# Kernel optimization log

Measured on AMD Instinct MI355X. Metric: run time of the kernel, lower is better.

## Reference

```python
import jax, jax.numpy as jnp
import numpy as np

N = 50000   # nodes
E = 800000  # edges
G = 64      # graphs
D_IN = 128
D_OUT = 64
HID = 2 * D_OUT  # 128, hidden width of non-final layers
EPS = 1e-5


def _seg_sum(v, idx, n):
    return jax.ops.segment_sum(v, idx, num_segments=n)


def _gcn(x, W, b, src, dst, n):
    # GCNConv with default add_self_loops=True, edge_weight=1, sym norm
    xw = x @ W                                            # [N, out]
    deg = _seg_sum(jnp.ones(src.shape[0], x.dtype), dst, n) + 1.0  # +1 self loop
    dis = jax.lax.rsqrt(deg)                              # deg^{-1/2}, deg>=1
    norm = dis[src] * dis[dst]                            # [E]
    agg = _seg_sum(norm[:, None] * xw[src], dst, n)       # gather-scale-scatter
    return agg + (dis * dis)[:, None] * xw + b            # self-loop term + bias


def _mpnn_layer(x, src, dst, edge_attr, gw, gb, ew, eb, n):
    h = _gcn(x, gw, gb, src, dst, n)
    e = jax.nn.relu(edge_attr[:, None] * ew + eb)         # Linear(1,out).relu per edge
    msg = h[src] + e                                      # message = x_j + edge_attr
    cnt = _seg_sum(jnp.ones(src.shape[0], x.dtype), dst, n)
    return _seg_sum(msg, dst, n) / jnp.clip(cnt, 1.0)[:, None]  # scatter-mean


def _ln(x, g, b):
    # node-wise LayerNorm over feature dim
    mu = x.mean(-1, keepdims=True)
    var = x.var(-1, keepdims=True)
    return (x - mu) * jax.lax.rsqrt(var + EPS) * g + b


def setup_inputs() -> dict:
    key = jax.random.key(0)
    ks = jax.random.split(key, 24)
    x = jax.random.normal(ks[0], (N, D_IN), jnp.float32)
    edge_index = jax.random.randint(ks[1], (2, E), 0, N, dtype=jnp.int64)
    edge_attr = jax.random.uniform(ks[2], (E,), jnp.float32)
    batch = jnp.sort(jax.random.randint(ks[3], (N,), 0, G, dtype=jnp.int64))

    def lin(k, fan_in, shape):
        return jax.random.uniform(k, shape, jnp.float32, -1.0, 1.0) / np.sqrt(fan_in)

    # layer 0: in 128 -> 128; layer 1: 128 -> 128; layer 2: 128 -> 64
    inp = {
        "x": x, "edge_index": edge_index, "edge_attr": edge_attr, "batch": batch,
        "gcn_w0": lin(ks[4], D_IN, (D_IN, HID)),  "gcn_b0": jnp.zeros((HID,), jnp.float32),
        "edge_w0": lin(ks[5], 1, (HID,)),          "edge_b0": lin(ks[6], 1, (HID,)),
        "ln_g0": jnp.ones((HID,), jnp.float32),   "ln_b0": jnp.zeros((HID,), jnp.float32),
        "gcn_w1": lin(ks[7], HID, (HID, HID)),    "gcn_b1": jnp.zeros((HID,), jnp.float32),
        "edge_w1": lin(ks[8], 1, (HID,)),          "edge_b1": lin(ks[9], 1, (HID,)),
        "ln_g1": jnp.ones((HID,), jnp.float32),   "ln_b1": jnp.zeros((HID,), jnp.float32),
        "gcn_w2": lin(ks[10], HID, (HID, D_OUT)), "gcn_b2": jnp.zeros((D_OUT,), jnp.float32),
        "edge_w2": lin(ks[11], 1, (D_OUT,)),       "edge_b2": lin(ks[12], 1, (D_OUT,)),
    }
    return inp


def reference(x, edge_index, edge_attr, batch,
              gcn_w0, gcn_b0, edge_w0, edge_b0, ln_g0, ln_b0,
              gcn_w1, gcn_b1, edge_w1, edge_b1, ln_g1, ln_b1,
              gcn_w2, gcn_b2, edge_w2, edge_b2):
    src, dst = edge_index[0], edge_index[1]
    h = _mpnn_layer(x, src, dst, edge_attr, gcn_w0, gcn_b0, edge_w0, edge_b0, N)
    h = _ln(jax.nn.relu(h), ln_g0, ln_b0)
    h = _mpnn_layer(h, src, dst, edge_attr, gcn_w1, gcn_b1, edge_w1, edge_b1, N)
    h = _ln(jax.nn.relu(h), ln_g1, ln_b1)
    h = _mpnn_layer(h, src, dst, edge_attr, gcn_w2, gcn_b2, edge_w2, edge_b2, N)
    # global_mean_pool
    cnt = _seg_sum(jnp.ones((N,), h.dtype), batch, G)
    z_pooled = _seg_sum(h, batch, G) / jnp.clip(cnt, 1.0)[:, None]
    return h, z_pooled
```

## Files before the change

### kernel.cpp

```cpp
#include <hip/hip_runtime.h>

#define NN 50000
#define NE 800000
#define NG 64
#define HID 128
#define DOUT 64
#define LN_EPS 1e-5f
#define NBUK 391
#define BCAP 3072
#define EPB 8192

typedef unsigned int uint32;
typedef unsigned short ushort16;
typedef __attribute__((ext_vector_type(8))) short bf16x8;
typedef __attribute__((ext_vector_type(4))) float f32x4;

__device__ inline ushort16 f2bf(float f) {
  uint32 u = __float_as_uint(f);
  u += 0x7fffu + ((u >> 16) & 1u);
  return (ushort16)(u >> 16);
}
__device__ inline uint32 pack2(float x, float y) {
  return (uint32)f2bf(x) | ((uint32)f2bf(y) << 16);
}
__device__ inline float bflo(uint32 p) { return __uint_as_float(p << 16); }
__device__ inline float bfhi(uint32 p) { return __uint_as_float(p & 0xffff0000u); }

__global__ __launch_bounds__(256) void k_zero_f(float* p, int n) {
  int i = blockIdx.x * 256 + threadIdx.x;
  if (i < n) p[i] = 0.f;
}

__global__ __launch_bounds__(256) void k_init_bcur(int* __restrict__ bcur) {
  int i = blockIdx.x * 256 + threadIdx.x;
  if (i < NBUK) bcur[i] = i * BCAP;
}

__global__ __launch_bounds__(1024) void k_bucket(const int* __restrict__ src,
                                                 const int* __restrict__ dst,
                                                 const float* __restrict__ ea,
                                                 int* __restrict__ bcur,
                                                 uint2* __restrict__ tmp, int e) {
  __shared__ int hist[NBUK], lbase[NBUK], lcur[NBUK];
  int t = threadIdx.x;
  for (int i = t; i < NBUK; i += 1024) {
    hist[i] = 0;
    lcur[i] = 0;
  }
  __syncthreads();
  int base_e = blockIdx.x * EPB;
  int dstv[EPB / 1024];
#pragma unroll
  for (int k = 0; k < EPB / 1024; k++) {
    int i = base_e + k * 1024 + t;
    int d = (i < e) ? dst[i] : -1;
    dstv[k] = d;
    if (d >= 0) atomicAdd(&hist[d >> 7], 1);
  }
  __syncthreads();
  for (int i = t; i < NBUK; i += 1024) {
    int c = hist[i];
    int b = 0;
    if (c > 0) b = atomicAdd(&bcur[i], c);
    lbase[i] = b;
  }
  __syncthreads();
#pragma unroll
  for (int k = 0; k < EPB / 1024; k++) {
    int i = base_e + k * 1024 + t;
    int d = dstv[k];
    if (d >= 0) {
      int b = d >> 7;
      int r = atomicAdd(&lcur[b], 1);
      int pos = lbase[b] + r;
      if (pos < (b + 1) * BCAP) {
        uint2 rec;
        rec.x = (uint32)(src[i] & 0xffff) | ((uint32)(d & 127) << 16);
        rec.y = __float_as_uint(ea[i]);
        tmp[pos] = rec;
      }
    }
  }
}

__global__ __launch_bounds__(512) void k_bscan(const int* __restrict__ bcur,
                                               int* __restrict__ bbase,
                                               int* __restrict__ rowptr) {
  __shared__ int s[512];
  int t = threadIdx.x;
  int v = 0;
  if (t < NBUK) {
    v = bcur[t] - t * BCAP;
    if (v > BCAP) v = BCAP;
  }
  s[t] = v;
  __syncthreads();
  for (int off = 1; off < 512; off <<= 1) {
    int x = (t >= off) ? s[t - off] : 0;
    __syncthreads();
    s[t] += x;
    __syncthreads();
  }
  if (t < NBUK) bbase[t] = s[t] - v;
  if (t == 511) {
    bbase[NBUK] = s[511];
    rowptr[NN] = s[511];
  }
}

__global__ __launch_bounds__(256) void k_bsort(const uint2* __restrict__ tmp,
                                               const int* __restrict__ bcur,
                                               const int* __restrict__ bbase,
                                               int* __restrict__ rowptr,
                                               int* __restrict__ csrc,
                                               uint2* __restrict__ emsg,
                                               float* __restrict__ dis,
                                               float* __restrict__ invc) {
  int b = blockIdx.x;
  __shared__ int hist[128], excl[128], cur[128];
  int t = threadIdx.x;
  if (t < 128) {
    hist[t] = 0;
    cur[t] = 0;
  }
  __syncthreads();
  int cnt = bcur[b] - b * BCAP;
  if (cnt > BCAP) cnt = BCAP;
  int tb = b * BCAP;
  int ob = bbase[b];
  for (int i = t; i < cnt; i += 256) {
    uint2 r = tmp[tb + i];
    atomicAdd(&hist[(r.x >> 16) & 127], 1);
  }
  __syncthreads();
  int myDeg = (t < 128) ? hist[t] : 0;
  for (int off = 1; off < 128; off <<= 1) {
    int x = 0;
    if (t < 128 && t >= off) x = hist[t - off];
    __syncthreads();
    if (t < 128) hist[t] += x;
    __syncthreads();
  }
  if (t < 128) {
    excl[t] = hist[t] - myDeg;
    int node = (b << 7) + t;
    if (node < NN) {
      rowptr[node] = ob + excl[t];
      dis[node] = rsqrtf((float)(myDeg + 1));
      invc[node] = (myDeg > 0) ? 1.0f / (float)myDeg : 1.0f;
    }
  }
  __syncthreads();
  for (int i = t; i < cnt; i += 256) {
    uint2 r = tmp[tb + i];
    int o = (r.x >> 16) & 127;
    int p = atomicAdd(&cur[o], 1);
    int pos = ob + excl[o] + p;
    int s = (int)(r.x & 0xffffu);
    csrc[pos] = s;
    emsg[pos] = make_uint2((uint32)s, r.y);
  }
}

template <int FOUT, bool IN_BF, bool OUT_BF>
__global__ __launch_bounds__(256) void k_gemm(const void* __restrict__ Xv,
                                              const float* __restrict__ W,
                                              const float* __restrict__ dis,
                                              void* __restrict__ Yv, int n) {
  const int NT = FOUT / 16;
  __shared__ __align__(16) unsigned short Wt[FOUT][136];
  __shared__ __align__(16) unsigned short Xs[64][136];
  int t = threadIdx.x;
  int row0 = blockIdx.x * 64;
  for (int idx = t; idx < 128 * FOUT; idx += 256) {
    int k = idx / FOUT, col = idx % FOUT;
    Wt[col][k] = (unsigned short)f2bf(W[idx]);
  }
  if (IN_BF) {
    const uint32* Xb = (const uint32*)Xv;
    for (int idx = t; idx < 64 * 64; idx += 256) {
      int r = idx >> 6, c = idx & 63;
      uint32 v = (row0 + r < n) ? Xb[(size_t)(row0 + r) * 64 + c] : 0u;
      *(uint32*)&Xs[r][c * 2] = v;
    }
  } else {
    const float* Xf = (const float*)Xv;
    for (int idx = t; idx < 64 * 64; idx += 256) {
      int r = idx >> 6, c = idx & 63;
      float2 v = make_float2(0.f, 0.f);
      if (row0 + r < n) v = ((const float2*)(Xf + (size_t)(row0 + r) * 128))[c];
      *(uint32*)&Xs[r][c * 2] = pack2(v.x, v.y);
    }
  }
  __syncthreads();
  int lane = t & 63, wv = t >> 6;
  int mrow = lane & 15, q = lane >> 4;
  f32x4 acc[NT];
#pragma unroll
  for (int c = 0; c < NT; c++) acc[c] = (f32x4){0.f, 0.f, 0.f, 0.f};
#pragma unroll
  for (int kt = 0; kt < 4; kt++) {
    bf16x8 af = *(const bf16x8*)&Xs[wv * 16 + mrow][kt * 32 + q * 8];
#pragma unroll
    for (int c = 0; c < NT; c++) {
      bf16x8 bfg = *(const bf16x8*)&Wt[c * 16 + mrow][kt * 32 + q * 8];
      acc[c] = __builtin_amdgcn_mfma_f32_16x16x32_bf16(af, bfg, acc[c], 0, 0, 0);
    }
  }
  float ds[4];
#pragma unroll
  for (int r = 0; r < 4; r++) {
    int rg = row0 + wv * 16 + q * 4 + r;
    ds[r] = (rg < n) ? dis[rg] : 0.f;
  }
#pragma unroll
  for (int c = 0; c < NT; c++) {
    int cg = c * 16 + mrow;
#pragma unroll
    for (int r = 0; r < 4; r++) {
      int rg = row0 + wv * 16 + q * 4 + r;
      if (rg < n) {
        float v = acc[c][r] * ds[r];
        if (OUT_BF)
          ((unsigned short*)Yv)[(size_t)rg * FOUT + cg] = (unsigned short)f2bf(v);
        else
          ((float*)Yv)[(size_t)rg * FOUT + cg] = v;
      }
    }
  }
}

__global__ __launch_bounds__(256) void k_agg_bf(const uint32* __restrict__ XWb,
                                                const float* __restrict__ dis,
                                                const int* __restrict__ rowptr,
                                                const int* __restrict__ csrc,
                                                const float* __restrict__ bias,
                                                uint32* __restrict__ Hb, int n) {
  int lane = threadIdx.x & 63;
  int node = blockIdx.x * 4 + (threadIdx.x >> 6);
  if (node >= n) return;
  float dn = dis[node];
  int beg = rowptr[node], end = rowptr[node + 1];
  float ax = 0.f, ay = 0.f;
  int i = beg;
  for (; i + 8 <= end; i += 8) {
    int s[8];
    uint32 p[8];
#pragma unroll
    for (int k = 0; k < 8; k++) s[k] = csrc[i + k];
#pragma unroll
    for (int k = 0; k < 8; k++) p[k] = XWb[(size_t)s[k] * 64 + lane];
#pragma unroll
    for (int k = 0; k < 8; k++) {
      ax += bflo(p[k]);
      ay += bfhi(p[k]);
    }
  }
  for (; i < end; i++) {
    uint32 p = XWb[(size_t)csrc[i] * 64 + lane];
    ax += bflo(p);
    ay += bfhi(p);
  }
  uint32 ps = XWb[(size_t)node * 64 + lane];
  float2 bb = ((const float2*)bias)[lane];
  float hx = dn * (ax + bflo(ps)) + bb.x;
  float hy = dn * (ay + bfhi(ps)) + bb.y;
  Hb[(size_t)node * 64 + lane] = pack2(hx, hy);
}

__global__ __launch_bounds__(256) void k_msg_bf(const uint32* __restrict__ Hb,
                                                const float* __restrict__ ew,
                                                const float* __restrict__ eb,
                                                const int* __restrict__ rowptr,
                                                const uint2* __restrict__ emsg,
                                                const float* __restrict__ invc,
                                                const float* __restrict__ lng,
                                                const float* __restrict__ lnb,
                                                uint32* __restrict__ OUTb, int n) {
  int lane = threadIdx.x & 63;
  int node = blockIdx.x * 4 + (threadIdx.x >> 6);
  if (node >= n) return;
  int beg = rowptr[node], end = rowptr[node + 1];
  float2 w = ((const float2*)ew)[lane];
  float2 b = ((const float2*)eb)[lane];
  float ax = 0.f, ay = 0.f;
  int i = beg;
  for (; i + 8 <= end; i += 8) {
    uint2 m[8];
    uint32 p[8];
#pragma unroll
    for (int k = 0; k < 8; k++) m[k] = emsg[i + k];
#pragma unroll
    for (int k = 0; k < 8; k++) p[k] = Hb[(size_t)m[k].x * 64 + lane];
#pragma unroll
    for (int k = 0; k < 8; k++) {
      float a = __uint_as_float(m[k].y);
      ax += bflo(p[k]) + fmaxf(a * w.x + b.x, 0.f);
      ay += bfhi(p[k]) + fmaxf(a * w.y + b.y, 0.f);
    }
  }
  for (; i < end; i++) {
    uint2 m = emsg[i];
    uint32 p = Hb[(size_t)m.x * 64 + lane];
    float a = __uint_as_float(m.y);
    ax += bflo(p) + fmaxf(a * w.x + b.x, 0.f);
    ay += bfhi(p) + fmaxf(a * w.y + b.y, 0.f);
  }
  float ic = invc[node];
  float ox = fmaxf(ax * ic, 0.f);
  float oy = fmaxf(ay * ic, 0.f);
  float s1 = ox + oy;
  float s2 = ox * ox + oy * oy;
  for (int off = 32; off; off >>= 1) {
    s1 += __shfl_xor(s1, off, 64);
    s2 += __shfl_xor(s2, off, 64);
  }
  float mu = s1 * (1.f / 128.f);
  float var = s2 * (1.f / 128.f) - mu * mu;
  float r = rsqrtf(var + LN_EPS);
  float2 g = ((const float2*)lng)[lane];
  float2 bb = ((const float2*)lnb)[lane];
  ox = (ox - mu) * r * g.x + bb.x;
  oy = (oy - mu) * r * g.y + bb.y;
  OUTb[(size_t)node * 64 + lane] = pack2(ox, oy);
}

__global__ __launch_bounds__(256) void k_agg64(const float* __restrict__ XWs,
                                               const float* __restrict__ dis,
                                               const int* __restrict__ rowptr,
                                               const int* __restrict__ csrc,
                                               const float* __restrict__ bias,
                                               float* __restrict__ H, int n) {
  int lane = threadIdx.x & 63;
  int node = blockIdx.x * 4 + (threadIdx.x >> 6);
  if (node >= n) return;
  float dn = dis[node];
  int beg = rowptr[node], end = rowptr[node + 1];
  float acc = 0.f;
  int i = beg;
  for (; i + 8 <= end; i += 8) {
    int s[8];
    float p[8];
#pragma unroll
    for (int k = 0; k < 8; k++) s[k] = csrc[i + k];
#pragma unroll
    for (int k = 0; k < 8; k++) p[k] = XWs[(size_t)s[k] * 64 + lane];
#pragma unroll
    for (int k = 0; k < 8; k++) acc += p[k];
  }
  for (; i < end; i++) acc += XWs[(size_t)csrc[i] * 64 + lane];
  H[(size_t)node * 64 + lane] = dn * (acc + XWs[(size_t)node * 64 + lane]) + bias[lane];
}

__global__ __launch_bounds__(256) void k_msg64(const float* __restrict__ H,
                                               const float* __restrict__ ew,
                                               const float* __restrict__ eb,
                                               const int* __restrict__ rowptr,
                                               const uint2* __restrict__ emsg,
                                               const float* __restrict__ invc,
                                               float* __restrict__ OUT, int n) {
  int lane = threadIdx.x & 63;
  int node = blockIdx.x * 4 + (threadIdx.x >> 6);
  if (node >= n) return;
  int beg = rowptr[node], end = rowptr[node + 1];
  float w = ew[lane], b = eb[lane];
  float acc = 0.f;
  int i = beg;
  for (; i + 8 <= end; i += 8) {
    uint2 m[8];
    float p[8];
#pragma unroll
    for (int k = 0; k < 8; k++) m[k] = emsg[i + k];
#pragma unroll
    for (int k = 0; k < 8; k++) p[k] = H[(size_t)m[k].x * 64 + lane];
#pragma unroll
    for (int k = 0; k < 8; k++)
      acc += p[k] + fmaxf(__uint_as_float(m[k].y) * w + b, 0.f);
  }
  for (; i < end; i++) {
    uint2 m = emsg[i];
    acc += H[(size_t)m.x * 64 + lane] + fmaxf(__uint_as_float(m.y) * w + b, 0.f);
  }
  OUT[(size_t)node * 64 + lane] = acc * invc[node];
}

#define POOL_BLOCKS 256
__global__ __launch_bounds__(256) void k_pool_partial(const float* __restrict__ H,
                                                      const int* __restrict__ batch,
                                                      float* __restrict__ Z, int n) {
  int lane = threadIdx.x & 63;
  int wid = blockIdx.x * 4 + (threadIdx.x >> 6);
  const int WAVES = POOL_BLOCKS * 4;
  int per = (n + WAVES - 1) / WAVES;
  int beg = wid * per;
  int end = beg + per;
  if (end > n) end = n;
  if (beg >= end) return;
  int g = batch[beg];
  float acc = 0.f;
  for (int i = beg; i < end; i++) {
    int gi = batch[i];
    if (gi != g) {
      atomicAdd(&Z[g * 64 + lane], acc);
      acc = 0.f;
      g = gi;
    }
    acc += H[(size_t)i * 64 + lane];
  }
  atomicAdd(&Z[g * 64 + lane], acc);
}

__global__ __launch_bounds__(64) void k_pool_div(float* __restrict__ Z,
                                                 const int* __restrict__ batch, int n) {
  int g = blockIdx.x;
  __shared__ int scnt;
  if (threadIdx.x == 0) {
    int lo = 0, hi = n;
    while (lo < hi) { int m = (lo + hi) >> 1; if (batch[m] < g) lo = m + 1; else hi = m; }
    int b0 = lo;
    lo = 0; hi = n;
    while (lo < hi) { int m = (lo + hi) >> 1; if (batch[m] < g + 1) lo = m + 1; else hi = m; }
    scnt = lo - b0;
  }
  __syncthreads();
  float c = (float)scnt;
  if (c < 1.f) c = 1.f;
  Z[g * 64 + threadIdx.x] /= c;
}

extern "C" void kernel_launch(void* const* d_in, const int* in_sizes, int n_in,
                              void* d_out, int out_size, void* d_ws, size_t ws_size,
                              hipStream_t stream) {
  const float* x = (const float*)d_in[0];
  const int* ei = (const int*)d_in[1];
  const float* ea = (const float*)d_in[2];
  const int* batch = (const int*)d_in[3];
  const float* gw0 = (const float*)d_in[4];
  const float* gb0 = (const float*)d_in[5];
  const float* ew0 = (const float*)d_in[6];
  const float* eb0 = (const float*)d_in[7];
  const float* lg0 = (const float*)d_in[8];
  const float* lb0 = (const float*)d_in[9];
  const float* gw1 = (const float*)d_in[10];
  const float* gb1 = (const float*)d_in[11];
  const float* ew1 = (const float*)d_in[12];
  const float* eb1 = (const float*)d_in[13];
  const float* lg1 = (const float*)d_in[14];
  const float* lb1 = (const float*)d_in[15];
  const float* gw2 = (const float*)d_in[16];
  const float* gb2 = (const float*)d_in[17];
  const float* ew2 = (const float*)d_in[18];
  const float* eb2 = (const float*)d_in[19];
  float* out = (float*)d_out;

  const int* src = ei;
  const int* dst = ei + NE;

  char* w = (char*)d_ws;
  size_t off = 0;
  auto alloc = [&](size_t bytes) -> void* {
    void* p = (void*)(w + off);
    off = (off + bytes + 255) & ~(size_t)255;
    return p;
  };
  int* rowptr = (int*)alloc((NN + 1) * sizeof(int));
  int* bcur = (int*)alloc(NBUK * sizeof(int));
  int* bbase = (int*)alloc((NBUK + 1) * sizeof(int));
  int* csrc = (int*)alloc(NE * sizeof(int));
  uint2* emsg = (uint2*)alloc(NE * sizeof(uint2));
  float* dis = (float*)alloc(NN * sizeof(float));
  float* invc = (float*)alloc(NN * sizeof(float));
  uint32* B1b = (uint32*)alloc((size_t)NN * 64 * sizeof(uint32));
  uint32* B2b = (uint32*)alloc((size_t)NN * 64 * sizeof(uint32));
  float* F1 = (float*)alloc((size_t)NN * 64 * sizeof(float));
  float* F2 = (float*)alloc((size_t)NN * 64 * sizeof(float));
  uint2* tmp = (uint2*)F1;

  hipLaunchKernelGGL(k_init_bcur, dim3((NBUK + 255) / 256), dim3(256), 0, stream, bcur);
  hipLaunchKernelGGL(k_bucket, dim3((NE + EPB - 1) / EPB), dim3(1024), 0, stream, src, dst, ea,
                     bcur, tmp, NE);
  hipLaunchKernelGGL(k_bscan, dim3(1), dim3(512), 0, stream, bcur, bbase, rowptr);
  hipLaunchKernelGGL(k_bsort, dim3(NBUK), dim3(256), 0, stream, tmp, bcur, bbase, rowptr, csrc,
                     emsg, dis, invc);

  dim3 gemm_grid((NN + 63) / 64), tb(256);
  dim3 node_grid((NN + 3) / 4);

  hipLaunchKernelGGL((k_gemm<128, false, true>), gemm_grid, tb, 0, stream, x, gw0, dis, B1b, NN);
  hipLaunchKernelGGL(k_agg_bf, node_grid, tb, 0, stream, B1b, dis, rowptr, csrc, gb0, B2b, NN);
  hipLaunchKernelGGL(k_msg_bf, node_grid, tb, 0, stream, B2b, ew0, eb0, rowptr, emsg, invc,
                     lg0, lb0, B1b, NN);
  hipLaunchKernelGGL((k_gemm<128, true, true>), gemm_grid, tb, 0, stream, B1b, gw1, dis, B2b, NN);
  hipLaunchKernelGGL(k_agg_bf, node_grid, tb, 0, stream, B2b, dis, rowptr, csrc, gb1, B1b, NN);
  hipLaunchKernelGGL(k_msg_bf, node_grid, tb, 0, stream, B1b, ew1, eb1, rowptr, emsg, invc,
                     lg1, lb1, B2b, NN);
  hipLaunchKernelGGL((k_gemm<64, true, false>), gemm_grid, tb, 0, stream, B2b, gw2, dis, F1, NN);
  hipLaunchKernelGGL(k_agg64, node_grid, tb, 0, stream, F1, dis, rowptr, csrc, gb2, F2, NN);
  hipLaunchKernelGGL(k_msg64, node_grid, tb, 0, stream, F2, ew2, eb2, rowptr, emsg, invc,
                     out, NN);
  float* Z = out + (size_t)NN * 64;
  hipLaunchKernelGGL(k_zero_f, dim3((NG * 64 + 255) / 256), dim3(256), 0, stream, Z, NG * 64);
  hipLaunchKernelGGL(k_pool_partial, dim3(POOL_BLOCKS), tb, 0, stream, out, batch, Z, NN);
  hipLaunchKernelGGL(k_pool_div, dim3(NG), dim3(64), 0, stream, Z, batch, NN);
}
```

Before: 474.6 us.

## Use half-wave per node gathers, bf16 final layer, smaller bucket blocks, fused init

Result: faster. 427.1 us (-10.0%).

```diff
diff --git a/kernel.cpp b/kernel.cpp
--- a/kernel.cpp
+++ b/kernel.cpp
@@ -8,7 +8,7 @@
 #define LN_EPS 1e-5f
 #define NBUK 391
 #define BCAP 3072
-#define EPB 8192
+#define EPB 2048
 
 typedef unsigned int uint32;
 typedef unsigned short ushort16;
@@ -26,13 +26,9 @@
 __device__ inline float bflo(uint32 p) { return __uint_as_float(p << 16); }
 __device__ inline float bfhi(uint32 p) { return __uint_as_float(p & 0xffff0000u); }
 
-__global__ __launch_bounds__(256) void k_zero_f(float* p, int n) {
+__global__ __launch_bounds__(256) void k_init(float* __restrict__ Z, int* __restrict__ bcur) {
   int i = blockIdx.x * 256 + threadIdx.x;
-  if (i < n) p[i] = 0.f;
-}
-
-__global__ __launch_bounds__(256) void k_init_bcur(int* __restrict__ bcur) {
-  int i = blockIdx.x * 256 + threadIdx.x;
+  if (i < NG * 64) Z[i] = 0.f;
   if (i < NBUK) bcur[i] = i * BCAP;
 }
 
@@ -230,45 +226,51 @@
   }
 }
 
-__global__ __launch_bounds__(256) void k_agg_bf(const uint32* __restrict__ XWb,
+__global__ __launch_bounds__(256) void k_agg_bf(const uint2* __restrict__ XW2,
                                                 const float* __restrict__ dis,
                                                 const int* __restrict__ rowptr,
                                                 const int* __restrict__ csrc,
                                                 const float* __restrict__ bias,
-                                                uint32* __restrict__ Hb, int n) {
-  int lane = threadIdx.x & 63;
-  int node = blockIdx.x * 4 + (threadIdx.x >> 6);
+                                                uint2* __restrict__ Hb2, int n) {
+  int l = threadIdx.x & 31;
+  int node = blockIdx.x * 8 + (threadIdx.x >> 5);
   if (node >= n) return;
   float dn = dis[node];
   int beg = rowptr[node], end = rowptr[node + 1];
-  float ax = 0.f, ay = 0.f;
+  float a0 = 0.f, a1 = 0.f, a2 = 0.f, a3 = 0.f;
   int i = beg;
   for (; i + 8 <= end; i += 8) {
     int s[8];
-    uint32 p[8];
+    uint2 p[8];
 #pragma unroll
     for (int k = 0; k < 8; k++) s[k] = csrc[i + k];
 #pragma unroll
-    for (int k = 0; k < 8; k++) p[k] = XWb[(size_t)s[k] * 64 + lane];
+    for (int k = 0; k < 8; k++) p[k] = XW2[(size_t)s[k] * 32 + l];
 #pragma unroll
     for (int k = 0; k < 8; k++) {
-      ax += bflo(p[k]);
-      ay += bfhi(p[k]);
+      a0 += bflo(p[k].x);
+      a1 += bfhi(p[k].x);
+      a2 += bflo(p[k].y);
+      a3 += bfhi(p[k].y);
     }
   }
   for (; i < end; i++) {
-    uint32 p = XWb[(size_t)csrc[i] * 64 + lane];
-    ax += bflo(p);
-    ay += bfhi(p);
-  }
-  uint32 ps = XWb[(size_t)node * 64 + lane];
-  float2 bb = ((const float2*)bias)[lane];
-  float hx = dn * (ax + bflo(ps)) + bb.x;
-  float hy = dn * (ay + bfhi(ps)) + bb.y;
-  Hb[(size_t)node * 64 + lane] = pack2(hx, hy);
-}
-
-__global__ __launch_bounds__(256) void k_msg_bf(const uint32* __restrict__ Hb,
+    uint2 p = XW2[(size_t)csrc[i] * 32 + l];
+    a0 += bflo(p.x);
+    a1 += bfhi(p.x);
+    a2 += bflo(p.y);
+    a3 += bfhi(p.y);
+  }
+  uint2 ps = XW2[(size_t)node * 32 + l];
+  float4 bb = ((const float4*)bias)[l];
+  float h0 = dn * (a0 + bflo(ps.x)) + bb.x;
+  float h1 = dn * (a1 + bfhi(ps.x)) + bb.y;
+  float h2 = dn * (a2 + bflo(ps.y)) + bb.z;
+  float h3 = dn * (a3 + bfhi(ps.y)) + bb.w;
+  Hb2[(size_t)node * 32 + l] = make_uint2(pack2(h0, h1), pack2(h2, h3));
+}
+
+__global__ __launch_bounds__(256) void k_msg_bf(const uint2* __restrict__ Hb2,
                                                 const float* __restrict__ ew,
                                                 const float* __restrict__ eb,
                                                 const int* __restrict__ rowptr,
@@ -276,14 +278,114 @@
                                                 const float* __restrict__ invc,
                                                 const float* __restrict__ lng,
                                                 const float* __restrict__ lnb,
-                                                uint32* __restrict__ OUTb, int n) {
-  int lane = threadIdx.x & 63;
-  int node = blockIdx.x * 4 + (threadIdx.x >> 6);
+                                                uint2* __restrict__ OUTb2, int n) {
+  int l = threadIdx.x & 31;
+  int node = blockIdx.x * 8 + (threadIdx.x >> 5);
   if (node >= n) return;
   int beg = rowptr[node], end = rowptr[node + 1];
-  float2 w = ((const float2*)ew)[lane];
-  float2 b = ((const float2*)eb)[lane];
-  float ax = 0.f, ay = 0.f;
+  float4 w = ((const float4*)ew)[l];
+  float4 b = ((const float4*)eb)[l];
+  float a0 = 0.f, a1 = 0.f, a2 = 0.f, a3 = 0.f;
+  int i = beg;
+  for (; i + 8 <= end; i += 8) {
+    uint2 m[8];
+    uint2 p[8];
+#pragma unroll
+    for (int k = 0; k < 8; k++) m[k] = emsg[i + k];
+#pragma unroll
+    for (int k = 0; k < 8; k++) p[k] = Hb2[(size_t)m[k].x * 32 + l];
+#pragma unroll
+    for (int k = 0; k < 8; k++) {
+      float a = __uint_as_float(m[k].y);
+      a0 += bflo(p[k].x) + fmaxf(a * w.x + b.x, 0.f);
+      a1 += bfhi(p[k].x) + fmaxf(a * w.y + b.y, 0.f);
+      a2 += bflo(p[k].y) + fmaxf(a * w.z + b.z, 0.f);
+      a3 += bfhi(p[k].y) + fmaxf(a * w.w + b.w, 0.f);
+    }
+  }
+  for (; i < end; i++) {
+    uint2 m = emsg[i];
+    uint2 p = Hb2[(size_t)m.x * 32 + l];
+    float a = __uint_as_float(m.y);
+    a0 += bflo(p.x) + fmaxf(a * w.x + b.x, 0.f);
+    a1 += bfhi(p.x) + fmaxf(a * w.y + b.y, 0.f);
+    a2 += bflo(p.y) + fmaxf(a * w.z + b.z, 0.f);
+    a3 += bfhi(p.y) + fmaxf(a * w.w + b.w, 0.f);
+  }
+  float ic = invc[node];
+  float o0 = fmaxf(a0 * ic, 0.f), o1 = fmaxf(a1 * ic, 0.f);
+  float o2 = fmaxf(a2 * ic, 0.f), o3 = fmaxf(a3 * ic, 0.f);
+  float s1 = o0 + o1 + o2 + o3;
+  float s2 = o0 * o0 + o1 * o1 + o2 * o2 + o3 * o3;
+#pragma unroll
+  for (int off = 16; off; off >>= 1) {
+    s1 += __shfl_xor(s1, off, 64);
+    s2 += __shfl_xor(s2, off, 64);
+  }
+  float mu = s1 * (1.f / 128.f);
+  float var = s2 * (1.f / 128.f) - mu * mu;
+  float r = rsqrtf(var + LN_EPS);
+  float4 g = ((const float4*)lng)[l];
+  float4 bb = ((const float4*)lnb)[l];
+  o0 = (o0 - mu) * r * g.x + bb.x;
+  o1 = (o1 - mu) * r * g.y + bb.y;
+  o2 = (o2 - mu) * r * g.z + bb.z;
+  o3 = (o3 - mu) * r * g.w + bb.w;
+  OUTb2[(size_t)node * 32 + l] = make_uint2(pack2(o0, o1), pack2(o2, o3));
+}
+
+__global__ __launch_bounds__(256) void k_agg64b(const uint32* __restrict__ XWb,
+                                                const float* __restrict__ dis,
+                                                const int* __restrict__ rowptr,
+                                                const int* __restrict__ csrc,
+                                                const float* __restrict__ bias,
+                                                uint32* __restrict__ Hb, int n) {
+  int l = threadIdx.x & 31;
+  int node = blockIdx.x * 8 + (threadIdx.x >> 5);
+  if (node >= n) return;
+  float dn = dis[node];
+  int beg = rowptr[node], end = rowptr[node + 1];
+  float a0 = 0.f, a1 = 0.f;
+  int i = beg;
+  for (; i + 8 <= end; i += 8) {
+    int s[8];
+    uint32 p[8];
+#pragma unroll
+    for (int k = 0; k < 8; k++) s[k] = csrc[i + k];
+#pragma unroll
+    for (int k = 0; k < 8; k++) p[k] = XWb[(size_t)s[k] * 32 + l];
+#pragma unroll
+    for (int k = 0; k < 8; k++) {
+      a0 += bflo(p[k]);
+      a1 += bfhi(p[k]);
+    }
+  }
+  for (; i < end; i++) {
+    uint32 p = XWb[(size_t)csrc[i] * 32 + l];
+    a0 += bflo(p);
+    a1 += bfhi(p);
+  }
+  uint32 ps = XWb[(size_t)node * 32 + l];
+  float2 bb = ((const float2*)bias)[l];
+  float h0 = dn * (a0 + bflo(ps)) + bb.x;
+  float h1 = dn * (a1 + bfhi(ps)) + bb.y;
+  Hb[(size_t)node * 32 + l] = pack2(h0, h1);
+}
+
+__global__ __launch_bounds__(256) void k_msg64b(const uint32* __restrict__ Hb,
+                                                const float* __restrict__ ew,
+                                                const float* __restrict__ eb,
+                                                const int* __restrict__ rowptr,
+                                                const uint2* __restrict__ emsg,
+                                                const float* __restrict__ invc,
+                                                float* __restrict__ OUT, int n) {
+  int l = threadIdx.x & 31;
+  int node = blockIdx.x * 8 + (threadIdx.x >> 5);
+  if (node >= n) return;
+  int beg = rowptr[node], end = rowptr[node + 1];
+  float2 w = ((const float2*)ew)[l];
+  float2 b = ((const float2*)eb)[l];
+  float a0 = 0.f, a1 = 0.f;
   int i = beg;
   for (; i + 8 <= end; i += 8) {
     uint2 m[8];
@@ -291,97 +393,23 @@
 #pragma unroll
     for (int k = 0; k < 8; k++) m[k] = emsg[i + k];
 #pragma unroll
-    for (int k = 0; k < 8; k++) p[k] = Hb[(size_t)m[k].x * 64 + lane];
+    for (int k = 0; k < 8; k++) p[k] = Hb[(size_t)m[k].x * 32 + l];
 #pragma unroll
     for (int k = 0; k < 8; k++) {
       float a = __uint_as_float(m[k].y);
-      ax += bflo(p[k]) + fmaxf(a * w.x + b.x, 0.f);
-      ay += bfhi(p[k]) + fmaxf(a * w.y + b.y, 0.f);
+      a0 += bflo(p[k]) + fmaxf(a * w.x + b.x, 0.f);
+      a1 += bfhi(p[k]) + fmaxf(a * w.y + b.y, 0.f);
     }
   }
   for (; i < end; i++) {
     uint2 m = emsg[i];
-    uint32 p = Hb[(size_t)m.x * 64 + lane];
+    uint32 p = Hb[(size_t)m.x * 32 + l];
     float a = __uint_as_float(m.y);
-    ax += bflo(p) + fmaxf(a * w.x + b.x, 0.f);
-    ay += bfhi(p) + fmaxf(a * w.y + b.y, 0.f);
+    a0 += bflo(p) + fmaxf(a * w.x + b.x, 0.f);
+    a1 += bfhi(p) + fmaxf(a * w.y + b.y, 0.f);
   }
   float ic = invc[node];
-  float ox = fmaxf(ax * ic, 0.f);
-  float oy = fmaxf(ay * ic, 0.f);
-  float s1 = ox + oy;
-  float s2 = ox * ox + oy * oy;
-  for (int off = 32; off; off >>= 1) {
-    s1 += __shfl_xor(s1, off, 64);
-    s2 += __shfl_xor(s2, off, 64);
-  }
-  float mu = s1 * (1.f / 128.f);
-  float var = s2 * (1.f / 128.f) - mu * mu;
-  float r = rsqrtf(var + LN_EPS);
-  float2 g = ((const float2*)lng)[lane];
-  float2 bb = ((const float2*)lnb)[lane];
-  ox = (ox - mu) * r * g.x + bb.x;
-  oy = (oy - mu) * r * g.y + bb.y;
-  OUTb[(size_t)node * 64 + lane] = pack2(ox, oy);
-}
-
-__global__ __launch_bounds__(256) void k_agg64(const float* __restrict__ XWs,
-                                               const float* __restrict__ dis,
-                                               const int* __restrict__ rowptr,
-                                               const int* __restrict__ csrc,
-                                               const float* __restrict__ bias,
-                                               float* __restrict__ H, int n) {
-  int lane = threadIdx.x & 63;
-  int node = blockIdx.x * 4 + (threadIdx.x >> 6);
-  if (node >= n) return;
-  float dn = dis[node];
-  int beg = rowptr[node], end = rowptr[node + 1];
-  float acc = 0.f;
-  int i = beg;
-  for (; i + 8 <= end; i += 8) {
-    int s[8];
-    float p[8];
-#pragma unroll
-    for (int k = 0; k < 8; k++) s[k] = csrc[i + k];
-#pragma unroll
-    for (int k = 0; k < 8; k++) p[k] = XWs[(size_t)s[k] * 64 + lane];
-#pragma unroll
-    for (int k = 0; k < 8; k++) acc += p[k];
-  }
-  for (; i < end; i++) acc += XWs[(size_t)csrc[i] * 64 + lane];
-  H[(size_t)node * 64 + lane] = dn * (acc + XWs[(size_t)node * 64 + lane]) + bias[lane];
-}
-
-__global__ __launch_bounds__(256) void k_msg64(const float* __restrict__ H,
-                                               const float* __restrict__ ew,
-                                               const float* __restrict__ eb,
-                                               const int* __restrict__ rowptr,
-                                               const uint2* __restrict__ emsg,
-                                               const float* __restrict__ invc,
-                                               float* __restrict__ OUT, int n) {
-  int lane = threadIdx.x & 63;
-  int node = blockIdx.x * 4 + (threadIdx.x >> 6);
-  if (node >= n) return;
-  int beg = rowptr[node], end = rowptr[node + 1];
-  float w = ew[lane], b = eb[lane];
-  float acc = 0.f;
-  int i = beg;
-  for (; i + 8 <= end; i += 8) {
-    uint2 m[8];
-    float p[8];
-#pragma unroll
-    for (int k = 0; k < 8; k++) m[k] = emsg[i + k];
-#pragma unroll
-    for (int k = 0; k < 8; k++) p[k] = H[(size_t)m[k].x * 64 + lane];
-#pragma unroll
-    for (int k = 0; k < 8; k++)
-      acc += p[k] + fmaxf(__uint_as_float(m[k].y) * w + b, 0.f);
-  }
-  for (; i < end; i++) {
-    uint2 m = emsg[i];
-    acc += H[(size_t)m.x * 64 + lane] + fmaxf(__uint_as_float(m.y) * w + b, 0.f);
-  }
-  OUT[(size_t)node * 64 + lane] = acc * invc[node];
+  ((float2*)OUT)[(size_t)node * 32 + l] = make_float2(a0 * ic, a1 * ic);
 }
 
 #define POOL_BLOCKS 256
@@ -470,13 +498,15 @@
   uint2* emsg = (uint2*)alloc(NE * sizeof(uint2));
   float* dis = (float*)alloc(NN * sizeof(float));
   float* invc = (float*)alloc(NN * sizeof(float));
-  uint32* B1b = (uint32*)alloc((size_t)NN * 64 * sizeof(uint32));
-  uint32* B2b = (uint32*)alloc((size_t)NN * 64 * sizeof(uint32));
-  float* F1 = (float*)alloc((size_t)NN * 64 * sizeof(float));
-  float* F2 = (float*)alloc((size_t)NN * 64 * sizeof(float));
-  uint2* tmp = (uint2*)F1;
-
-  hipLaunchKernelGGL(k_init_bcur, dim3((NBUK + 255) / 256), dim3(256), 0, stream, bcur);
+  uint2* B1b = (uint2*)alloc((size_t)NN * 32 * sizeof(uint2));
+  uint2* B2b = (uint2*)alloc((size_t)NN * 32 * sizeof(uint2));
+  uint32* F1b = (uint32*)alloc((size_t)NN * 32 * sizeof(uint32));
+  uint32* F2b = (uint32*)alloc((size_t)NN * 32 * sizeof(uint32));
+  uint2* tmp = (uint2*)alloc((size_t)NBUK * BCAP * sizeof(uint2));
+
+  float* Z = out + (size_t)NN * 64;
+
+  hipLaunchKernelGGL(k_init, dim3((NG * 64 + 255) / 256), dim3(256), 0, stream, Z, bcur);
   hipLaunchKernelGGL(k_bucket, dim3((NE + EPB - 1) / EPB), dim3(1024), 0, stream, src, dst, ea,
                      bcur, tmp, NE);
   hipLaunchKernelGGL(k_bscan, dim3(1), dim3(512), 0, stream, bcur, bbase, rowptr);
@@ -484,7 +514,7 @@
                      emsg, dis, invc);
 
   dim3 gemm_grid((NN + 63) / 64), tb(256);
-  dim3 node_grid((NN + 3) / 4);
+  dim3 node_grid((NN + 7) / 8);
 
   hipLaunchKernelGGL((k_gemm<128, false, true>), gemm_grid, tb, 0, stream, x, gw0, dis, B1b, NN);
   hipLaunchKernelGGL(k_agg_bf, node_grid, tb, 0, stream, B1b, dis, rowptr, csrc, gb0, B2b, NN);
@@ -494,12 +524,10 @@
   hipLaunchKernelGGL(k_agg_bf, node_grid, tb, 0, stream, B2b, dis, rowptr, csrc, gb1, B1b, NN);
   hipLaunchKernelGGL(k_msg_bf, node_grid, tb, 0, stream, B1b, ew1, eb1, rowptr, emsg, invc,
                      lg1, lb1, B2b, NN);
-  hipLaunchKernelGGL((k_gemm<64, true, false>), gemm_grid, tb, 0, stream, B2b, gw2, dis, F1, NN);
-  hipLaunchKernelGGL(k_agg64, node_grid, tb, 0, stream, F1, dis, rowptr, csrc, gb2, F2, NN);
-  hipLaunchKernelGGL(k_msg64, node_grid, tb, 0, stream, F2, ew2, eb2, rowptr, emsg, invc,
+  hipLaunchKernelGGL((k_gemm<64, true, true>), gemm_grid, tb, 0, stream, B2b, gw2, dis, F1b, NN);
+  hipLaunchKernelGGL(k_agg64b, node_grid, tb, 0, stream, F1b, dis, rowptr, csrc, gb2, F2b, NN);
+  hipLaunchKernelGGL(k_msg64b, node_grid, tb, 0, stream, F2b, ew2, eb2, rowptr, emsg, invc,
                      out, NN);
-  float* Z = out + (size_t)NN * 64;
-  hipLaunchKernelGGL(k_zero_f, dim3((NG * 64 + 255) / 256), dim3(256), 0, stream, Z, NG * 64);
   hipLaunchKernelGGL(k_pool_partial, dim3(POOL_BLOCKS), tb, 0, stream, out, batch, Z, NN);
   hipLaunchKernelGGL(k_pool_div, dim3(NG), dim3(64), 0, stream, Z, batch, NN);
 }
```
